# Kernel optimization log

Measured on AMD Instinct MI355X. Metric: run time of the kernel, lower is better.

The kernel has to match this reference:

```python
import jax, jax.numpy as jnp
import numpy as np

H = 16
D_MODEL = 1024
D_K = D_MODEL // H


def setup_inputs() -> dict:
    key = jax.random.key(0)
    ks = jax.random.split(key, 12)
    B, S = 2, 2048
    scale = 1.0 / np.sqrt(D_MODEL)
    inp = {
        "query": jax.random.normal(ks[0], (B, S, D_MODEL), jnp.float32),
        "key": jax.random.normal(ks[1], (B, S, D_MODEL), jnp.float32),
        "value": jax.random.normal(ks[2], (B, S, D_MODEL), jnp.float32),
        "mask": jnp.ones((B, 1, S), jnp.int32),
        "Wq": jax.random.normal(ks[3], (D_MODEL, D_MODEL), jnp.float32) * scale,
        "bq": jnp.zeros((D_MODEL,), jnp.float32),
        "Wk": jax.random.normal(ks[4], (D_MODEL, D_MODEL), jnp.float32) * scale,
        "bk": jnp.zeros((D_MODEL,), jnp.float32),
        "Wv": jax.random.normal(ks[5], (D_MODEL, D_MODEL), jnp.float32) * scale,
        "bv": jnp.zeros((D_MODEL,), jnp.float32),
        "Wo": jax.random.normal(ks[6], (D_MODEL, D_MODEL), jnp.float32) * scale,
        "bo": jnp.zeros((D_MODEL,), jnp.float32),
    }
    return inp


def reference(query, key, value, mask, Wq, bq, Wk, bk, Wv, bv, Wo, bo):
    B, S, _ = query.shape
    # QKV projections, split heads: [B, S, D] -> [B, H, S, d_k]
    def proj(x, W, b):
        y = x @ W.T + b
        return y.reshape(B, -1, H, D_K).transpose(0, 2, 1, 3)

    q = proj(query, Wq, bq)
    k = proj(key, Wk, bk)
    v = proj(value, Wv, bv)

    # scaled dot-product attention with full score matrix [B, H, Sq, Sk]
    scores = jnp.einsum("bhqd,bhkd->bhqk", q, k) / np.sqrt(D_K)
    m = mask[:, None, :, :]  # unsqueeze head dim: [B, 1, 1_or_S, S]
    scores = jnp.where(m == 0, jnp.float32(-1e9), scores)
    p_attn = jax.nn.softmax(scores, axis=-1)  # dropout p=0.0 (eval)
    x = jnp.einsum("bhqk,bhkd->bhqd", p_attn, v)

    # merge heads and output projection
    x = x.transpose(0, 2, 1, 3).reshape(B, -1, H * D_K)
    return x @ Wo.T + bo
```

## Files before the change

### kernel.cpp

```cpp
#include <hip/hip_runtime.h>
#include <hip/hip_bf16.h>
#include <stdint.h>

typedef unsigned short us;
typedef __bf16 bf8 __attribute__((ext_vector_type(8)));
typedef float  f4  __attribute__((ext_vector_type(4)));

typedef unsigned int __attribute__((address_space(1))) as1_uint;
typedef unsigned int __attribute__((address_space(3))) as3_uint;

__device__ __forceinline__ void async_ld16(const void* g, void* l) {
    __builtin_amdgcn_global_load_lds((as1_uint*)g, (as3_uint*)l, 16, 0, 0);
}

__device__ __forceinline__ us f2bf(float f) {
    __hip_bfloat16 h = __float2bfloat16(f);
    us u;
    __builtin_memcpy(&u, &h, 2);
    return u;
}

__device__ __forceinline__ float fexp2(float x) {
#if __has_builtin(__builtin_amdgcn_exp2f)
    return __builtin_amdgcn_exp2f(x);
#else
    return exp2f(x);
#endif
}

#define SCALE_Q 0.18033688011112042f

__global__ __launch_bounds__(256)
void convert_all(const float* __restrict__ s0, const float* __restrict__ s1,
                 const float* __restrict__ s2, const float* __restrict__ s3,
                 const float* __restrict__ s4, const float* __restrict__ s5,
                 const float* __restrict__ s6,
                 us* __restrict__ d0, us* __restrict__ d1, us* __restrict__ d2,
                 us* __restrict__ d3, us* __restrict__ d4, us* __restrict__ d5,
                 us* __restrict__ d6)
{
    size_t i4 = (((size_t)blockIdx.x * 256) + threadIdx.x) << 2;
    const float* src; us* dst; size_t off;
    if (i4 < ((size_t)3 << 22)) {
        unsigned seg = (unsigned)(i4 >> 22);
        off = i4 & (((size_t)1 << 22) - 1);
        src = seg == 0 ? s0 : (seg == 1 ? s1 : s2);
        dst = seg == 0 ? d0 : (seg == 1 ? d1 : d2);
    } else {
        size_t j = i4 - ((size_t)3 << 22);
        unsigned seg = (unsigned)(j >> 20);
        off = j & (((size_t)1 << 20) - 1);
        src = seg == 0 ? s3 : (seg == 1 ? s4 : (seg == 2 ? s5 : s6));
        dst = seg == 0 ? d3 : (seg == 1 ? d4 : (seg == 2 ? d5 : d6));
    }
    float4 f = *(const float4*)(src + off);
    ushort4 o;
    o.x = f2bf(f.x); o.y = f2bf(f.y); o.z = f2bf(f.z); o.w = f2bf(f.w);
    *(ushort4*)(dst + off) = o;
}

template<int MODE, int BN>
__device__ __forceinline__
void gemm_body(const us* __restrict__ A, const us* __restrict__ W,
               const float* __restrict__ bias, void* __restrict__ out,
               float scale, int bx, int by)
{
    __shared__ us lA[128 * 32];
    __shared__ us lB[BN * 32];

    const int tid  = threadIdx.x;
    const int wv   = tid >> 6;
    const int lane = tid & 63;
    const int l15  = lane & 15;
    const int quad = lane >> 4;
    const int kq   = quad << 3;
    const int cr   = quad << 2;
    const int srow = lane >> 2;
    const int scol = (lane & 3) << 3;
    const int m0   = by << 7;
    const int n0   = bx * BN;
    constexpr int MJ = (BN == 128) ? 4 : 2;
    const int wm = (BN == 128) ? ((wv >> 1) << 6) : (wv << 5);
    const int wn = (BN == 128) ? ((wv & 1) << 6) : 0;

    f4 acc[4][MJ];
    const f4 zero = {0.f, 0.f, 0.f, 0.f};
#pragma unroll
    for (int i = 0; i < 4; ++i)
#pragma unroll
        for (int j = 0; j < MJ; ++j) acc[i][j] = zero;

    for (int kt = 0; kt < 1024; kt += 32) {
#pragma unroll
        for (int s = 0; s < 2; ++s) {
            const int chunk = wv * 2 + s;
            const int row   = chunk * 16 + srow;
            async_ld16(A + (size_t)(m0 + row) * 1024 + kt + scol, &lA[chunk * 512]);
        }
        if (BN == 128) {
#pragma unroll
            for (int s = 0; s < 2; ++s) {
                const int chunk = wv * 2 + s;
                const int row   = chunk * 16 + srow;
                async_ld16(W + (size_t)(n0 + row) * 1024 + kt + scol, &lB[chunk * 512]);
            }
        } else {
            const int row = wv * 16 + srow;
            async_ld16(W + (size_t)(n0 + row) * 1024 + kt + scol, &lB[wv * 512]);
        }
        __syncthreads();

        bf8 wf[4], xf[MJ];
#pragma unroll
        for (int i = 0; i < 4; ++i)
            wf[i] = *(const bf8*)&lB[(wn + i * 16 + l15) * 32 + kq];
#pragma unroll
        for (int j = 0; j < MJ; ++j)
            xf[j] = *(const bf8*)&lA[(wm + j * 16 + l15) * 32 + kq];
#pragma unroll
        for (int i = 0; i < 4; ++i)
#pragma unroll
            for (int j = 0; j < MJ; ++j)
                acc[i][j] = __builtin_amdgcn_mfma_f32_16x16x32_bf16(wf[i], xf[j], acc[i][j], 0, 0, 0);
        __syncthreads();
    }

    if (MODE == 2) {
        us* o = (us*)out;
#pragma unroll
        for (int j = 0; j < MJ; ++j) {
            const int f = m0 + wm + j * 16 + l15;
            const float bf_ = bias[f];
            const int hh = f >> 6, dd = f & 63;
#pragma unroll
            for (int i = 0; i < 4; ++i) {
                const int tokb = n0 + wn + i * 16 + cr;
                const int bb = tokb >> 11, ss = tokb & 2047;
                us hp[4];
#pragma unroll
                for (int r = 0; r < 4; ++r) hp[r] = f2bf(acc[i][j][r] + bf_);
                uint2 w;
                w.x = (unsigned)hp[0] | ((unsigned)hp[1] << 16);
                w.y = (unsigned)hp[2] | ((unsigned)hp[3] << 16);
                *(uint2*)&o[((size_t)((bb * 16 + hh) * 64 + dd) << 11) + ss] = w;
            }
        }
        return;
    }

#pragma unroll
    for (int i = 0; i < 4; ++i) {
        const int gnb = n0 + wn + i * 16 + cr;
        const f4 bj = *(const f4*)&bias[gnb];
        if (MODE == 0) {
            us* o = (us*)out;
            const int hh = gnb >> 6, dd = gnb & 63;
#pragma unroll
            for (int j = 0; j < MJ; ++j) {
                const int gm = m0 + wm + j * 16 + l15;
                const int bb = gm >> 11, ss = gm & 2047;
                us hp[4];
#pragma unroll
                for (int r = 0; r < 4; ++r)
                    hp[r] = f2bf((acc[i][j][r] + bj[r]) * scale);
                uint2 w;
                w.x = (unsigned)hp[0] | ((unsigned)hp[1] << 16);
                w.y = (unsigned)hp[2] | ((unsigned)hp[3] << 16);
                *(uint2*)&o[(((size_t)(bb * 16 + hh) * 2048 + ss) << 6) + dd] = w;
            }
        } else {
            float* o = (float*)out;
#pragma unroll
            for (int j = 0; j < MJ; ++j) {
                const int gm = m0 + wm + j * 16 + l15;
                f4 v;
#pragma unroll
                for (int r = 0; r < 4; ++r) v[r] = acc[i][j][r] + bj[r];
                *(f4*)&o[((size_t)gm << 10) + gnb] = v;
            }
        }
    }
}

__global__ __launch_bounds__(256)
void gemm_qkv(const us* __restrict__ XQ, const us* __restrict__ XK,
              const us* __restrict__ XV,
              const us* __restrict__ WQ, const us* __restrict__ WK,
              const us* __restrict__ WV,
              const float* __restrict__ bq, const float* __restrict__ bk,
              const float* __restrict__ bv,
              us* __restrict__ QP, us* __restrict__ KP, us* __restrict__ VT)
{
    const int z = blockIdx.z;
    if (z == 2) {
        gemm_body<2, 128>(WV, XV, bv, VT, 1.0f, blockIdx.y, blockIdx.x);
        return;
    }
    const us* A = z == 0 ? XQ : XK;
    const us* W = z == 0 ? WQ : WK;
    const float* b = z == 0 ? bq : bk;
    us* o = z == 0 ? QP : KP;
    const float scale = z == 0 ? SCALE_Q : 1.0f;
    gemm_body<0, 128>(A, W, b, o, scale, blockIdx.x, blockIdx.y);
}

__global__ __launch_bounds__(256)
void gemm_o(const us* __restrict__ A, const us* __restrict__ W,
            const float* __restrict__ bias, float* __restrict__ out)
{
    gemm_body<1, 64>(A, W, bias, out, 1.0f, blockIdx.x, blockIdx.y);
}

__global__ __launch_bounds__(256)
void flash_attn(const us* __restrict__ Qp, const us* __restrict__ Kp,
                const us* __restrict__ Vtp, const int* __restrict__ maskp,
                us* __restrict__ ctx)
{
    __shared__ us lK[2][64 * 64];
    __shared__ us lVt[2][64 * 64];
    __shared__ us lP[4 * 32 * 72];
    __shared__ float lmask[2][64];

    const int tid  = threadIdx.x;
    const int wv   = tid >> 6;
    const int lane = tid & 63;
    const int l15  = lane & 15;
    const int quad = lane >> 4;
    const int cr   = quad << 2;
    const int l7   = l15 & 7;

    const int q0 = blockIdx.x << 7;
    const int h  = blockIdx.y;
    const int b  = blockIdx.z;

    const size_t headoff = ((size_t)(b * 16 + h)) << 17;
    const us* Qh  = Qp  + headoff;
    const us* Kh  = Kp  + headoff;
    const us* Vth = Vtp + headoff;

    const int gr    = lane >> 3;
    const int gslot = ((lane & 7) ^ gr) << 3;

    bf8 qf[2][2];
#pragma unroll
    for (int nt = 0; nt < 2; ++nt)
#pragma unroll
        for (int kb = 0; kb < 2; ++kb)
            qf[nt][kb] = *(const bf8*)(Qh + ((size_t)(q0 + wv * 32 + nt * 16 + l15) << 6)
                                          + kb * 32 + (quad << 3));

    const f4 zero = {0.f, 0.f, 0.f, 0.f};
    f4 of[4][2];
#pragma unroll
    for (int dt = 0; dt < 4; ++dt)
#pragma unroll
        for (int nt = 0; nt < 2; ++nt) of[dt][nt] = zero;
    float li[2] = {0.f, 0.f};

    us* lPw = lP + wv * (32 * 72);

#define FA_ISSUE(kt0, bi)                                                      \
    {                                                                          \
        _Pragma("unroll")                                                      \
        for (int i = 0; i < 2; ++i) {                                          \
            const int rbase = wv * 16 + i * 8;                                 \
            const int r = rbase + gr;                                          \
            async_ld16(Kh + ((size_t)((kt0) + r) << 6) + gslot,                \
                       &lK[bi][rbase * 64]);                                   \
            async_ld16(Vth + (size_t)r * 2048 + (kt0) + gslot,                 \
                       &lVt[bi][rbase * 64]);                                  \
        }                                                                      \
        if (tid < 64)                                                          \
            lmask[bi][tid] =                                                   \
                (maskp[((size_t)b << 11) + (kt0) + tid] == 0) ? 0.0f : 1.0f;   \
    }

    FA_ISSUE(0, 0);

    for (int t = 0; t < 32; ++t) {
        const int cur = t & 1;
        __syncthreads();
        if (t < 31) FA_ISSUE((t + 1) * 64, cur ^ 1);

        const us* lKc  = lK[cur];
        const us* lVtc = lVt[cur];

        float rs[2] = {0.f, 0.f};
#pragma unroll
        for (int kt = 0; kt < 4; ++kt) {
            const int krow = (kt * 16 + l15) << 6;
            bf8 kf0 = *(const bf8*)&lKc[krow + ((quad ^ l7) << 3)];
            bf8 kf1 = *(const bf8*)&lKc[krow + (((4 + quad) ^ l7) << 3)];
            f4 st[2];
#pragma unroll
            for (int nt = 0; nt < 2; ++nt) {
                st[nt] = __builtin_amdgcn_mfma_f32_16x16x32_bf16(kf0, qf[nt][0], zero, 0, 0, 0);
                st[nt] = __builtin_amdgcn_mfma_f32_16x16x32_bf16(kf1, qf[nt][1], st[nt], 0, 0, 0);
            }
            const f4 mr = *(const f4*)&lmask[cur][kt * 16 + cr];
#pragma unroll
            for (int nt = 0; nt < 2; ++nt) {
                us hp[4];
#pragma unroll
                for (int r = 0; r < 4; ++r) {
                    const float p = fexp2(st[nt][r]) * mr[r];
                    rs[nt] += p;
                    hp[r] = f2bf(p);
                }
                uint2 w;
                w.x = (unsigned)hp[0] | ((unsigned)hp[1] << 16);
                w.y = (unsigned)hp[2] | ((unsigned)hp[3] << 16);
                *(uint2*)&lPw[(nt * 16 + l15) * 72 + kt * 16 + cr] = w;
            }
        }
#pragma unroll
        for (int nt = 0; nt < 2; ++nt) {
            float r2 = rs[nt];
            r2 += __shfl_xor(r2, 16, 64);
            r2 += __shfl_xor(r2, 32, 64);
            li[nt] += r2;
        }

#pragma unroll
        for (int kb = 0; kb < 2; ++kb) {
            bf8 pfr[2];
#pragma unroll
            for (int nt = 0; nt < 2; ++nt)
                pfr[nt] = *(const bf8*)&lPw[(nt * 16 + l15) * 72 + kb * 32 + (quad << 3)];
#pragma unroll
            for (int dt = 0; dt < 4; ++dt) {
                bf8 vf = *(const bf8*)&lVtc[((dt * 16 + l15) << 6) + (((kb * 4 + quad) ^ l7) << 3)];
#pragma unroll
                for (int nt = 0; nt < 2; ++nt)
                    of[dt][nt] = __builtin_amdgcn_mfma_f32_16x16x32_bf16(vf, pfr[nt], of[dt][nt], 0, 0, 0);
            }
        }
    }
#undef FA_ISSUE

#pragma unroll
    for (int nt = 0; nt < 2; ++nt) {
        const float linv = 1.0f / li[nt];
        const int tok = q0 + wv * 32 + nt * 16 + l15;
        const size_t rowb = (((size_t)(b * 2048 + tok)) << 10) + (h << 6);
#pragma unroll
        for (int dt = 0; dt < 4; ++dt) {
            us hp[4];
#pragma unroll
            for (int r = 0; r < 4; ++r) hp[r] = f2bf(of[dt][nt][r] * linv);
            uint2 w;
            w.x = (unsigned)hp[0] | ((unsigned)hp[1] << 16);
            w.y = (unsigned)hp[2] | ((unsigned)hp[3] << 16);
            *(uint2*)&ctx[rowb + dt * 16 + cr] = w;
        }
    }
}

extern "C" void kernel_launch(void* const* d_in, const int* in_sizes, int n_in,
                              void* d_out, int out_size, void* d_ws, size_t ws_size,
                              hipStream_t stream)
{
    const float* q    = (const float*)d_in[0];
    const float* k    = (const float*)d_in[1];
    const float* v    = (const float*)d_in[2];
    const int*   mask = (const int*)d_in[3];
    const float* Wq   = (const float*)d_in[4];
    const float* bq   = (const float*)d_in[5];
    const float* Wk   = (const float*)d_in[6];
    const float* bk   = (const float*)d_in[7];
    const float* Wv   = (const float*)d_in[8];
    const float* bv   = (const float*)d_in[9];
    const float* Wo   = (const float*)d_in[10];
    const float* bo   = (const float*)d_in[11];
    float* out = (float*)d_out;

    us* ws  = (us*)d_ws;
    us* XQ  = ws;
    us* XK  = ws + 4194304;
    us* XV  = ws + 8388608;
    us* WQb = ws + 12582912;
    us* WKb = ws + 13631488;
    us* WVb = ws + 14680064;
    us* WOb = ws + 15728640;
    us* QP  = ws + 16777216;
    us* KP  = ws + 20971520;
    us* VT  = ws + 25165824;
    us* CTX = XQ;

    convert_all<<<16384, 256, 0, stream>>>(q, k, v, Wq, Wk, Wv, Wo,
                                           XQ, XK, XV, WQb, WKb, WVb, WOb);
    gemm_qkv<<<dim3(8, 32, 3), 256, 0, stream>>>(XQ, XK, XV, WQb, WKb, WVb,
                                                 bq, bk, bv, QP, KP, VT);
    flash_attn<<<dim3(16, 16, 2), 256, 0, stream>>>(QP, KP, VT, mask, CTX);
    gemm_o<<<dim3(16, 32), 256, 0, stream>>>(CTX, WOb, bo, out);
}
```

Measured before the change: 248.2 us.

## Split flash attention over two KV halves and merge with a combine kernel

```diff
diff --git a/kernel.cpp b/kernel.cpp
--- a/kernel.cpp
+++ b/kernel.cpp
@@ -211,10 +211,12 @@
     gemm_body<1, 64>(A, W, bias, out, 1.0f, blockIdx.x, blockIdx.y);
 }
 
+template<int SPLIT>
 __global__ __launch_bounds__(256)
 void flash_attn(const us* __restrict__ Qp, const us* __restrict__ Kp,
                 const us* __restrict__ Vtp, const int* __restrict__ maskp,
-                us* __restrict__ ctx)
+                us* __restrict__ ctx, float* __restrict__ OP,
+                float* __restrict__ LI)
 {
     __shared__ us lK[2][64 * 64];
     __shared__ us lVt[2][64 * 64];
@@ -231,7 +233,11 @@
 
     const int q0 = blockIdx.x << 7;
     const int h  = blockIdx.y;
-    const int b  = blockIdx.z;
+    const int bz = blockIdx.z;
+    const int b   = SPLIT ? (bz >> 1) : bz;
+    const int kvh = SPLIT ? (bz & 1) : 0;
+    constexpr int NT = SPLIT ? 16 : 32;
+    const int ktbase = kvh << 10;
 
     const size_t headoff = ((size_t)(b * 16 + h)) << 17;
     const us* Qh  = Qp  + headoff;
@@ -275,12 +281,12 @@
                 (maskp[((size_t)b << 11) + (kt0) + tid] == 0) ? 0.0f : 1.0f;   \
     }
 
-    FA_ISSUE(0, 0);
-
-    for (int t = 0; t < 32; ++t) {
+    FA_ISSUE(ktbase, 0);
+
+    for (int t = 0; t < NT; ++t) {
         const int cur = t & 1;
         __syncthreads();
-        if (t < 31) FA_ISSUE((t + 1) * 64, cur ^ 1);
+        if (t < NT - 1) FA_ISSUE(ktbase + (t + 1) * 64, cur ^ 1);
 
         const us* lKc  = lK[cur];
         const us* lVtc = lVt[cur];
@@ -338,22 +344,58 @@
     }
 #undef FA_ISSUE
 
-#pragma unroll
-    for (int nt = 0; nt < 2; ++nt) {
-        const float linv = 1.0f / li[nt];
-        const int tok = q0 + wv * 32 + nt * 16 + l15;
-        const size_t rowb = (((size_t)(b * 2048 + tok)) << 10) + (h << 6);
-#pragma unroll
-        for (int dt = 0; dt < 4; ++dt) {
-            us hp[4];
-#pragma unroll
-            for (int r = 0; r < 4; ++r) hp[r] = f2bf(of[dt][nt][r] * linv);
-            uint2 w;
-            w.x = (unsigned)hp[0] | ((unsigned)hp[1] << 16);
-            w.y = (unsigned)hp[2] | ((unsigned)hp[3] << 16);
-            *(uint2*)&ctx[rowb + dt * 16 + cr] = w;
-        }
-    }
+    if constexpr (SPLIT) {
+        float* op = OP + ((size_t)kvh << 22);
+#pragma unroll
+        for (int nt = 0; nt < 2; ++nt) {
+            const int tok = q0 + wv * 32 + nt * 16 + l15;
+            if (quad == 0)
+                LI[(((size_t)(kvh * 2 + b) * 16 + h) << 11) + tok] = li[nt];
+            const size_t rowb = (((size_t)(b * 2048 + tok)) << 10) + (h << 6);
+#pragma unroll
+            for (int dt = 0; dt < 4; ++dt)
+                *(f4*)&op[rowb + dt * 16 + cr] = of[dt][nt];
+        }
+    } else {
+#pragma unroll
+        for (int nt = 0; nt < 2; ++nt) {
+            const float linv = 1.0f / li[nt];
+            const int tok = q0 + wv * 32 + nt * 16 + l15;
+            const size_t rowb = (((size_t)(b * 2048 + tok)) << 10) + (h << 6);
+#pragma unroll
+            for (int dt = 0; dt < 4; ++dt) {
+                us hp[4];
+#pragma unroll
+                for (int r = 0; r < 4; ++r) hp[r] = f2bf(of[dt][nt][r] * linv);
+                uint2 w;
+                w.x = (unsigned)hp[0] | ((unsigned)hp[1] << 16);
+                w.y = (unsigned)hp[2] | ((unsigned)hp[3] << 16);
+                *(uint2*)&ctx[rowb + dt * 16 + cr] = w;
+            }
+        }
+    }
+}
+
+__global__ __launch_bounds__(256)
+void combine_o(const float* __restrict__ OP, const float* __restrict__ LI,
+               us* __restrict__ ctx)
+{
+    size_t i4 = (((size_t)blockIdx.x * 256) + threadIdx.x) << 2;
+    const unsigned f   = (unsigned)(i4 & 1023);
+    const unsigned tok = (unsigned)((i4 >> 10) & 2047);
+    const unsigned b   = (unsigned)(i4 >> 21);
+    const unsigned h   = f >> 6;
+    float4 o0 = *(const float4*)(OP + i4);
+    float4 o1 = *(const float4*)(OP + ((size_t)1 << 22) + i4);
+    const size_t lidx = (((size_t)b * 16 + h) << 11) + tok;
+    const float l = LI[lidx] + LI[(size_t)65536 + lidx];
+    const float linv = 1.0f / l;
+    ushort4 o;
+    o.x = f2bf((o0.x + o1.x) * linv);
+    o.y = f2bf((o0.y + o1.y) * linv);
+    o.z = f2bf((o0.z + o1.z) * linv);
+    o.w = f2bf((o0.w + o1.w) * linv);
+    *(ushort4*)&ctx[i4] = o;
 }
 
 extern "C" void kernel_launch(void* const* d_in, const int* in_sizes, int n_in,
@@ -386,11 +428,21 @@
     us* KP  = ws + 20971520;
     us* VT  = ws + 25165824;
     us* CTX = XQ;
+    float* OP = (float*)(ws + 29360128);
+    float* LI = (float*)(ws + 46137344);
+    const bool split = (ws_size >= 92798976);
 
     convert_all<<<16384, 256, 0, stream>>>(q, k, v, Wq, Wk, Wv, Wo,
                                            XQ, XK, XV, WQb, WKb, WVb, WOb);
     gemm_qkv<<<dim3(8, 32, 3), 256, 0, stream>>>(XQ, XK, XV, WQb, WKb, WVb,
                                                  bq, bk, bv, QP, KP, VT);
-    flash_attn<<<dim3(16, 16, 2), 256, 0, stream>>>(QP, KP, VT, mask, CTX);
+    if (split) {
+        flash_attn<1><<<dim3(16, 16, 4), 256, 0, stream>>>(QP, KP, VT, mask,
+                                                           CTX, OP, LI);
+        combine_o<<<4096, 256, 0, stream>>>(OP, LI, CTX);
+    } else {
+        flash_attn<0><<<dim3(16, 16, 2), 256, 0, stream>>>(QP, KP, VT, mask,
+                                                           CTX, OP, LI);
+    }
     gemm_o<<<dim3(16, 32), 256, 0, stream>>>(CTX, WOb, bo, out);
 }
```

After: 252.9 us. About the same (+1.9%).
